# Kernel optimization log

Hardware: AMD Instinct MI355X
Metric: run time of the kernel (lower is better)

Reference implementation:

```python
import jax, jax.numpy as jnp
import numpy as np

E, H = 1024, 16


def setup_inputs() -> dict:
    key = jax.random.key(0)
    k1, k2, k3, k4 = jax.random.split(key, 4)
    B, L = 4, 2048
    embeddings = jax.random.normal(k1, (B, L, E), dtype=jnp.float32)
    mask = jax.random.randint(k2, (B, L, L), 0, 2) == 1  # True = masked out
    # Params (torch Linear y = x @ W.T; we store already-transposed [in, out])
    W_qkv = jax.random.normal(k3, (E, 3 * E), dtype=jnp.float32) * 0.02
    W_out = jax.random.normal(k4, (E, E), dtype=jnp.float32) * 0.02
    return {"embeddings": embeddings, "mask": mask, "W_qkv": W_qkv, "W_out": W_out}


def reference(embeddings, mask, W_qkv, W_out):
    B, L, E_ = embeddings.shape
    A = E_ // H
    scale = A ** (-0.5)
    qkv = embeddings @ W_qkv                       # [B, L, 3E]
    qkv = qkv.reshape(B, L, H, 3 * A).transpose(0, 2, 1, 3)  # [B, H, L, 3A]
    q, k, v = jnp.split(qkv, 3, axis=-1)           # each [B, H, L, A]
    scores = jnp.einsum('bhqa,bhka->bhqk', q, k) * scale  # [B, H, L, L]
    m = mask[:, None, :, :]                        # [B, 1, L, L]
    fully = jnp.all(m, axis=-1, keepdims=True)     # rows with every key masked
    scores = jnp.where(m, -jnp.inf, scores)
    scores = jnp.where(fully, 0.0, scores)         # keep softmax finite
    attn = jax.nn.softmax(scores, axis=-1)
    attn = jnp.where(fully, 0.0, attn)             # == torch nan_to_num(0)
    values = jnp.einsum('bhqk,bhka->bhqa', attn, v)  # [B, H, L, A]
    values = values.transpose(0, 2, 1, 3).reshape(B, L, E_)
    return values @ W_out
```

## Files before the change

### kernel.cpp

```cpp
#include <hip/hip_runtime.h>
#include <hip/hip_bf16.h>

#define B_   4
#define L_   2048
#define E_   1024
#define H_   16
#define T_   8192
#define K_   1024

typedef __attribute__((ext_vector_type(8))) short bf16x8;
typedef __attribute__((ext_vector_type(4))) float f32x4;
typedef __attribute__((ext_vector_type(4))) unsigned u32x4;

#define CSC_ (0.125f * 1.44269504f)

__device__ __forceinline__ ushort f2b(float f) {
    union { float f; unsigned u; } x; x.f = f;
    unsigned r = (x.u + 0x7fffu + ((x.u >> 16) & 1u)) >> 16;
    return (ushort)r;
}

__device__ __forceinline__ float fexp2(float x) {
#if __has_builtin(__builtin_amdgcn_exp2f)
    return __builtin_amdgcn_exp2f(x);
#else
    return __expf(x * 0.69314718056f);
#endif
}

__device__ __forceinline__ unsigned pack2bf(float a, float b) {
#if __has_builtin(__builtin_amdgcn_cvt_pk_bf16_f32)
    auto t = __builtin_amdgcn_cvt_pk_bf16_f32(a, b);
    return __builtin_bit_cast(unsigned, t);
#else
    unsigned ua = __builtin_bit_cast(unsigned, a) + 0x8000u;
    unsigned ub = __builtin_bit_cast(unsigned, b) + 0x8000u;
    return __builtin_amdgcn_perm(ub, ua, 0x07060302);
#endif
}

#define GLD_LDS16(gp, lp) __builtin_amdgcn_global_load_lds( \
    (const __attribute__((address_space(1))) void*)(gp), \
    (__attribute__((address_space(3))) void*)(lp), 16, 0, 0)

__global__ void detect_mask_layout(const unsigned char* __restrict__ m, int* flag) {
    __shared__ int s;
    if (threadIdx.x == 0) s = 0;
    __syncthreads();
    int found = 0;
    for (int i = threadIdx.x; i < 4096; i += 256)
        if ((i & 3) != 0 && m[i] != 0) found = 1;
    if (found) atomicOr(&s, 1);
    __syncthreads();
    if (threadIdx.x == 0) *flag = s;
}

__global__ void pack_mask(const void* __restrict__ mraw, const int* __restrict__ flag,
                          unsigned* __restrict__ tbits) {
    int row  = blockIdx.x;
    int lane = threadIdx.x & 63;
    int wave = threadIdx.x >> 6;
    int isByte = *flag;
    int b = row >> 11, q = row & 2047;
    const unsigned char* mb = (const unsigned char*)mraw;
    const int*           mi = (const int*)mraw;
    long long base = (long long)row * L_;
    for (int w = wave; w < 32; w += 4) {
        int idx = w * 64 + lane;
        int v = isByte ? (int)mb[base + idx] : mi[base + idx];
        unsigned long long word = __ballot(v == 0);
        if (lane == 0) {
            tbits[((size_t)b * 64 + 2 * w)     * 2048 + q] = (unsigned)word;
            tbits[((size_t)b * 64 + 2 * w + 1) * 2048 + q] = (unsigned)(word >> 32);
        }
    }
}

__global__ __launch_bounds__(256) void conv_bf16(const float* __restrict__ in,
                                                 ushort* __restrict__ out) {
    int i = blockIdx.x * 256 + threadIdx.x;
    float4 v = ((const float4*)in)[i];
    uint2 o;
    o.x = (unsigned)f2b(v.x) | ((unsigned)f2b(v.y) << 16);
    o.y = (unsigned)f2b(v.z) | ((unsigned)f2b(v.w) << 16);
    ((uint2*)out)[i] = o;
}

__global__ __launch_bounds__(256) void transpose_conv(const float* __restrict__ in,
        ushort* __restrict__ out, int R, int Cn) {
    __shared__ float t[32][33];
    int c0 = blockIdx.x * 32, r0 = blockIdx.y * 32;
    int x = threadIdx.x & 31, y = threadIdx.x >> 5;
#pragma unroll
    for (int k = 0; k < 4; ++k)
        t[y + k * 8][x] = in[(size_t)(r0 + y + k * 8) * Cn + c0 + x];
    __syncthreads();
#pragma unroll
    for (int k = 0; k < 4; ++k)
        out[(size_t)(c0 + y + k * 8) * R + r0 + x] = f2b(t[x][y + k * 8]);
}

template<int NDIM, int MODE>
__global__ __launch_bounds__(256, 4) void gemm_bf16(
        const ushort* __restrict__ Ab, const ushort* __restrict__ Bt,
        float* __restrict__ Cg, ushort* __restrict__ Qb,
        ushort* __restrict__ Kb, ushort* __restrict__ Vt) {
    __shared__ ushort As[2][128 * 32];
    __shared__ ushort Bs[2][128 * 32];
    const int tid = threadIdx.x;
    const int wv = tid >> 6, ln = tid & 63;
    const int bn = blockIdx.x * 128, bm = blockIdx.y * 128;
    const int wm = (wv & 1) * 64, wn = (wv >> 1) * 64;
    const int row16 = ln & 15, quad = ln >> 4;

    const int rr = ln >> 2;
    const int cc8 = (((ln & 3) ^ ((rr >> 1) & 3)) * 8);

    const ushort* Ag = Ab + (size_t)(bm + wv * 32 + rr) * K_ + cc8;
    const ushort* Bg = Bt + (size_t)(bn + wv * 32 + rr) * K_ + cc8;

    auto stage = [&](int k0, int buf) {
#pragma unroll
        for (int g = 0; g < 2; ++g) {
            GLD_LDS16(Ag + (size_t)(g * 16) * K_ + k0, &As[buf][(wv * 32 + g * 16) * 32]);
            GLD_LDS16(Bg + (size_t)(g * 16) * K_ + k0, &Bs[buf][(wv * 32 + g * 16) * 32]);
        }
    };

    f32x4 acc[4][4];
#pragma unroll
    for (int i = 0; i < 4; ++i)
#pragma unroll
        for (int j = 0; j < 4; ++j) acc[i][j] = (f32x4){0.f, 0.f, 0.f, 0.f};

    const int ch = (quad ^ ((row16 >> 1) & 3)) * 8;

    auto compute = [&](const ushort* Ac, const ushort* Bc) {
        bf16x8 af[4], bf[4];
#pragma unroll
        for (int i = 0; i < 4; ++i)
            af[i] = *(const bf16x8*)&Ac[(wm + i * 16 + row16) * 32 + ch];
#pragma unroll
        for (int j = 0; j < 4; ++j)
            bf[j] = *(const bf16x8*)&Bc[(wn + j * 16 + row16) * 32 + ch];
#pragma unroll
        for (int i = 0; i < 4; ++i)
#pragma unroll
            for (int j = 0; j < 4; ++j)
                acc[i][j] = __builtin_amdgcn_mfma_f32_16x16x32_bf16(
                    af[i], bf[j], acc[i][j], 0, 0, 0);
    };

    stage(0, 0);
    __syncthreads();

    for (int t = 0; t < 32; t += 2) {
        stage((t + 1) * 32, 1);
        compute(As[0], Bs[0]);
        __syncthreads();
        if (t + 2 < 32) stage((t + 2) * 32, 0);
        compute(As[1], Bs[1]);
        __syncthreads();
    }

    if (MODE == 0) {
#pragma unroll
        for (int i = 0; i < 4; ++i)
#pragma unroll
            for (int j = 0; j < 4; ++j) {
                int col = bn + wn + j * 16 + row16;
#pragma unroll
                for (int r = 0; r < 4; ++r) {
                    int row = bm + wm + i * 16 + quad * 4 + r;
                    Cg[(size_t)row * NDIM + col] = acc[i][j][r];
                }
            }
    } else {
#pragma unroll
        for (int j = 0; j < 4; ++j) {
            int col = bn + wn + j * 16 + row16;
            int h = col / 192, w = col - h * 192;
            int sel = w >> 6, a = w & 63;
            float qs = (sel == 0) ? CSC_ : 1.0f;
#pragma unroll
            for (int i = 0; i < 4; ++i)
#pragma unroll
                for (int r = 0; r < 4; ++r) {
                    int rowg = bm + wm + i * 16 + quad * 4 + r;
                    int b = rowg >> 11, l = rowg & 2047;
                    ushort v = f2b(acc[i][j][r] * qs);
                    size_t bh = (size_t)(b * H_ + h);
                    if (sel == 0)      Qb[(bh * L_ + l) * 64 + a] = v;
                    else if (sel == 1) Kb[(bh * L_ + l) * 64 + a] = v;
                    else {
                        int k5 = l & 31;
                        int lp = (l & ~31) | (2 * (k5 & 15) + (k5 >> 4));
                        Vt[(bh * 64 + a) * L_ + lp] = v;
                    }
                }
        }
    }
}

__global__ __launch_bounds__(512, 4) void attn_mfma(
        const ushort* __restrict__ Qb, const ushort* __restrict__ Kb,
        const ushort* __restrict__ Vt, const unsigned* __restrict__ tbits,
        ushort* __restrict__ vals) {
    __shared__ ushort KV[6][4096];

    const int tid = threadIdx.x, wv = tid >> 6, ln = tid & 63;
    const int bh = blockIdx.x, b = bh >> 4, h = bh & 15;
    const int q0 = blockIdx.y * 256;
    const int row16 = ln & 15, quad = ln >> 4;
    const int lh = ln >> 3, ll = ln & 7;
    const int cg8 = ((ll ^ lh) * 8);

    const ushort* Kg = Kb + (size_t)bh * L_ * 64;
    const ushort* Vg = Vt + (size_t)bh * 64 * L_;

    const int wk = wv & 3;
    const bool isK = (wv < 4);
    const int vc4 = ll ^ lh;
    const ushort* vstage = Vg + (size_t)(wk * 8 + lh + 32 * (vc4 >> 2)) * L_ + (vc4 & 3) * 8;
    const ushort* kstage = Kg + (size_t)(wk * 8 + lh) * 64 + cg8;

    ushort* lds = &KV[0][0];

    {
        const ushort* Qgw = Qb + ((size_t)bh * L_ + q0 + wv * 32) * 64;
#pragma unroll
        for (int it = 0; it < 4; ++it)
            GLD_LDS16(Qgw + (size_t)(it * 8 + lh) * 64 + cg8,
                      lds + (wv * 32 + it * 8) * 64);
    }
    __syncthreads();
    bf16x8 aq[2][2];
#pragma unroll
    for (int rg = 0; rg < 2; ++rg)
#pragma unroll
        for (int ks = 0; ks < 2; ++ks)
            aq[rg][ks] = *(const bf16x8*)&lds[(wv * 32 + rg * 16 + row16) * 64 +
                                              (((ks * 4 + quad) ^ (row16 & 7)) * 8)];
    __syncthreads();

    if (isK) {
        GLD_LDS16(kstage,               &KV[0][(wk * 8) * 64]);
        GLD_LDS16(kstage + 2048,        &KV[0][(32 + wk * 8) * 64]);
        GLD_LDS16(kstage + 4096,        &KV[1][(wk * 8) * 64]);
        GLD_LDS16(kstage + 4096 + 2048, &KV[1][(32 + wk * 8) * 64]);
        kstage += 8192;
    } else {
        GLD_LDS16(vstage,      &KV[3][(wk * 8) * 64]);
        GLD_LDS16(vstage + 32, &KV[3][(32 + wk * 8) * 64]);
        GLD_LDS16(vstage + 64, &KV[4][(wk * 8) * 64]);
        GLD_LDS16(vstage + 96, &KV[4][(32 + wk * 8) * 64]);
        vstage += 128;
    }

    bf16x8 vone;
#pragma unroll
    for (int i = 0; i < 8; ++i) vone[i] = (short)0x3F80;
    const f32x4 zf = (f32x4){0.f, 0.f, 0.f, 0.f};

    f32x4 oacc[2][4], lacc[2];
#pragma unroll
    for (int rg = 0; rg < 2; ++rg) {
        lacc[rg] = zf;
#pragma unroll
        for (int t = 0; t < 4; ++t) oacc[rg][t] = zf;
    }

    const unsigned* mptr = tbits + (size_t)b * 64 * 2048 + (q0 + wv * 32 + row16);

    auto qk = [&](const ushort* kbuf, int sub, f32x4 (&s)[2][2]) {
        __builtin_amdgcn_s_setprio(1);
#pragma unroll
        for (int ks = 0; ks < 2; ++ks) {
            bf16x8 bk[2];
#pragma unroll
            for (int t = 0; t < 2; ++t)
                bk[t] = *(const bf16x8*)&kbuf[(sub * 32 + t * 16 + row16) * 64 +
                                              (((ks * 4 + quad) ^ (row16 & 7)) * 8)];
#pragma unroll
            for (int rg = 0; rg < 2; ++rg)
#pragma unroll
                for (int t = 0; t < 2; ++t)
                    s[rg][t] = __builtin_amdgcn_mfma_f32_16x16x32_bf16(
                        bk[t], aq[rg][ks], ks ? s[rg][t] : zf, 0, 0, 0);
        }
        __builtin_amdgcn_s_setprio(0);
    };

    auto sm_pv = [&](f32x4 (&sa)[2][2], unsigned mlo, unsigned mhi,
                     const ushort* vbuf, int sub) {
        bf16x8 ap[2];
#pragma unroll
        for (int rg = 0; rg < 2; ++rg) {
            unsigned wr = rg ? mhi : mlo;
            u32x4 pw;
#pragma unroll
            for (int r = 0; r < 4; ++r) {
                unsigned sh = wr >> (quad * 4 + r);
                unsigned pk = pack2bf(fexp2(sa[rg][0][r]), fexp2(sa[rg][1][r]));
                pk &= (sh & 0x00010001u) * 0xFFFFu;
                pw[r] = pk;
            }
            ap[rg] = __builtin_bit_cast(bf16x8, pw);
        }
        bf16x8 bv[4];
#pragma unroll
        for (int t = 0; t < 4; ++t)
            bv[t] = *(const bf16x8*)&vbuf[(sub * 32 + (t & 1) * 16 + row16) * 64 +
                                          ((((t >> 1) * 4 + quad) ^ (row16 & 7)) * 8)];
        __builtin_amdgcn_s_setprio(1);
#pragma unroll
        for (int rg = 0; rg < 2; ++rg) {
            lacc[rg] = __builtin_amdgcn_mfma_f32_16x16x32_bf16(
                ap[rg], vone, lacc[rg], 0, 0, 0);
#pragma unroll
            for (int t = 0; t < 4; ++t)
                oacc[rg][t] = __builtin_amdgcn_mfma_f32_16x16x32_bf16(
                    ap[rg], bv[t], oacc[rg][t], 0, 0, 0);
        }
        __builtin_amdgcn_s_setprio(0);
    };

    auto iter = [&](const ushort* kb, const ushort* vb,
                    ushort* kn, ushort* vn, bool st) {
        unsigned m0lo = mptr[0],    m0hi = mptr[16];
        unsigned m1lo = mptr[2048], m1hi = mptr[2048 + 16];
        mptr += 4096;
        __builtin_amdgcn_sched_barrier(0);
        if (st) {
            if (isK) {
                GLD_LDS16(kstage,        kn + (wk * 8) * 64);
                GLD_LDS16(kstage + 2048, kn + (32 + wk * 8) * 64);
                kstage += 4096;
            } else {
                GLD_LDS16(vstage,      vn + (wk * 8) * 64);
                GLD_LDS16(vstage + 32, vn + (32 + wk * 8) * 64);
                vstage += 64;
            }
        }
        f32x4 s0[2][2];
        qk(kb, 0, s0);
        sm_pv(s0, m0lo, m0hi, vb, 0);
        f32x4 s1[2][2];
        qk(kb, 1, s1);
        sm_pv(s1, m1lo, m1hi, vb, 1);
        asm volatile("s_waitcnt vmcnt(2)" ::: "memory");
        __builtin_amdgcn_s_barrier();
        __builtin_amdgcn_sched_barrier(0);
    };

    asm volatile("s_waitcnt vmcnt(2)" ::: "memory");
    __builtin_amdgcn_s_barrier();
    __builtin_amdgcn_sched_barrier(0);

    for (int g = 0; g < 10; ++g) {
        iter(KV[0], KV[3], KV[2], KV[5], true);
        iter(KV[1], KV[4], KV[0], KV[3], true);
        iter(KV[2], KV[5], KV[1], KV[4], true);
    }
    iter(KV[0], KV[3], KV[2], KV[5], false);
    iter(KV[1], KV[4], KV[0], KV[3], false);

#pragma unroll
    for (int rg = 0; rg < 2; ++rg)
#pragma unroll
        for (int r = 0; r < 4; ++r) {
            float l = lacc[rg][r];
            float inv = (l > 0.f) ? 1.0f / l : 0.f;
            int qrow = q0 + wv * 32 + rg * 16 + quad * 4 + r;
            size_t base = ((size_t)b * L_ + qrow) * E_ + h * 64;
#pragma unroll
            for (int t = 0; t < 4; ++t)
                vals[base + t * 16 + row16] = f2b(oacc[rg][t][r] * inv);
        }
}

extern "C" void kernel_launch(void* const* d_in, const int* in_sizes, int n_in,
                              void* d_out, int out_size, void* d_ws, size_t ws_size,
                              hipStream_t stream) {
    const float* emb  = (const float*)d_in[0];
    const void*  mask = d_in[1];
    const float* wqkv = (const float*)d_in[2];
    const float* wout = (const float*)d_in[3];
    float* out = (float*)d_out;

    char* ws = (char*)d_ws;
    const size_t NEED = 4096ull + 2097152ull + 2ull * 46137344ull;
    if (ws_size < NEED) return;

    int* flag = (int*)ws;
    unsigned* tbits = (unsigned*)(ws + 4096);
    ushort* embb  = (ushort*)(ws + 4096 + 2097152);
    ushort* Wqkvt = embb  + 8388608;
    ushort* Wott  = Wqkvt + 3145728;
    ushort* Qb    = Wott  + 1048576;
    ushort* Kb    = Qb    + 8388608;
    ushort* Vt    = Kb    + 8388608;
    ushort* vals  = Vt    + 8388608;

    detect_mask_layout<<<1, 256, 0, stream>>>((const unsigned char*)mask, flag);
    pack_mask<<<T_, 256, 0, stream>>>(mask, flag, tbits);
    conv_bf16<<<8192, 256, 0, stream>>>(emb, embb);
    transpose_conv<<<dim3(96, 32), 256, 0, stream>>>(wqkv, Wqkvt, 1024, 3072);
    transpose_conv<<<dim3(32, 32), 256, 0, stream>>>(wout, Wott, 1024, 1024);
    gemm_bf16<3072, 1><<<dim3(24, 64), 256, 0, stream>>>(
        embb, Wqkvt, nullptr, Qb, Kb, Vt);
    attn_mfma<<<dim3(64, 8), 512, 0, stream>>>(Qb, Kb, Vt, tbits, vals);
    gemm_bf16<1024, 0><<<dim3(8, 64), 256, 0, stream>>>(
        vals, Wott, out, nullptr, nullptr, nullptr);
}
```

Measured before the change: 351.3 us.

## Add dedicated 256x256-tile QKV GEMM with fine-grained load/MFMA interleaving

```diff
diff --git a/kernel.cpp b/kernel.cpp
--- a/kernel.cpp
+++ b/kernel.cpp
@@ -100,11 +100,143 @@
         out[(size_t)(c0 + y + k * 8) * R + r0 + x] = f2b(t[x][y + k * 8]);
 }
 
-template<int NDIM, int MODE>
+#define QAT_ 16384
+
+__global__ __launch_bounds__(512) void gemm_qkv(
+        const ushort* __restrict__ Ab, const ushort* __restrict__ Bt,
+        ushort* __restrict__ Qb, ushort* __restrict__ Kb,
+        ushort* __restrict__ Vt) {
+    __shared__ ushort Asb[2 * QAT_];
+    __shared__ ushort Bsb[2 * QAT_];
+
+    const int tid = threadIdx.x;
+    const int wv = tid >> 6, ln = tid & 63;
+    const int bn = blockIdx.x * 256, bm = blockIdx.y * 256;
+    const int wm = (wv & 1) * 128, wn = (wv >> 1) * 64;
+    const int row16 = ln & 15, quad = ln >> 4;
+    const int lh = ln >> 3, ll = ln & 7;
+    const int sw8 = (ll ^ lh) * 8;
+
+    auto stA = [&](int t, int q, ushort* dst) {
+        int r0 = 128 * (wv >> 2) + 32 * q + (wv & 3) * 8;
+        GLD_LDS16(Ab + (size_t)(bm + r0 + lh) * K_ + t * 64 + sw8,
+                  dst + r0 * 64);
+    };
+    auto stB = [&](int t, int r, ushort* dst) {
+        int r0 = 64 * r + wv * 8;
+        GLD_LDS16(Bt + (size_t)(bn + r0 + lh) * K_ + t * 64 + sw8,
+                  dst + r0 * 64);
+    };
+
+    f32x4 acc[8][4];
+#pragma unroll
+    for (int i = 0; i < 8; ++i)
+#pragma unroll
+        for (int j = 0; j < 4; ++j) acc[i][j] = (f32x4){0.f, 0.f, 0.f, 0.f};
+
+#pragma unroll
+    for (int q = 0; q < 4; ++q) stA(0, q, Asb);
+#pragma unroll
+    for (int r = 0; r < 4; ++r) stB(0, r, Bsb);
+#pragma unroll
+    for (int q = 0; q < 3; ++q) stA(1, q, Asb + QAT_);
+#pragma unroll
+    for (int r = 0; r < 3; ++r) stB(1, r, Bsb + QAT_);
+    asm volatile("s_waitcnt vmcnt(6)" ::: "memory");
+    __builtin_amdgcn_s_barrier();
+    __builtin_amdgcn_sched_barrier(0);
+
+    for (int i = 0; i < 8; ++i) {
+        bf16x8 bfr[4][2];
+#pragma unroll
+        for (int p = 0; p < 8; ++p) {
+            const int half = p >> 2, q = p & 3;
+            const ushort* Ar = Asb + half * QAT_;
+            const ushort* Br = Bsb + half * QAT_;
+            bf16x8 af[2][2];
+#pragma unroll
+            for (int di = 0; di < 2; ++di)
+#pragma unroll
+                for (int ks = 0; ks < 2; ++ks) {
+                    int row = wm + (2 * q + di) * 16 + row16;
+                    af[di][ks] = *(const bf16x8*)&Ar[row * 64 +
+                                     (((ks * 4 + quad) ^ (row16 & 7)) * 8)];
+                }
+            if (q == 0) {
+#pragma unroll
+                for (int j = 0; j < 4; ++j)
+#pragma unroll
+                    for (int ks = 0; ks < 2; ++ks) {
+                        int row = wn + j * 16 + row16;
+                        bfr[j][ks] = *(const bf16x8*)&Br[row * 64 +
+                                         (((ks * 4 + quad) ^ (row16 & 7)) * 8)];
+                    }
+            }
+            if (p == 0) {
+                stA(2 * i + 1, 3, Asb + QAT_);
+                stB(2 * i + 1, 3, Bsb + QAT_);
+            } else if (p <= 4) {
+                if (i < 7) { stA(2 * i + 2, p - 1, Asb);
+                             stB(2 * i + 2, p - 1, Bsb); }
+            } else {
+                if (i < 7) { stA(2 * i + 3, p - 5, Asb + QAT_);
+                             stB(2 * i + 3, p - 5, Bsb + QAT_); }
+            }
+            __builtin_amdgcn_sched_barrier(0);
+            __builtin_amdgcn_s_barrier();
+            asm volatile("s_waitcnt lgkmcnt(0)" ::: "memory");
+            __builtin_amdgcn_sched_barrier(0);
+            __builtin_amdgcn_s_setprio(1);
+#pragma unroll
+            for (int ks = 0; ks < 2; ++ks)
+#pragma unroll
+                for (int di = 0; di < 2; ++di)
+#pragma unroll
+                    for (int j = 0; j < 4; ++j)
+                        acc[2 * q + di][j] = __builtin_amdgcn_mfma_f32_16x16x32_bf16(
+                            af[di][ks], bfr[j][ks], acc[2 * q + di][j], 0, 0, 0);
+            __builtin_amdgcn_s_setprio(0);
+            if (p == 3) {
+                if (i < 7) { asm volatile("s_waitcnt vmcnt(6)" ::: "memory"); }
+                else       { asm volatile("s_waitcnt vmcnt(0)" ::: "memory"); }
+            }
+            if (p == 7 && i < 7) {
+                asm volatile("s_waitcnt vmcnt(6)" ::: "memory");
+            }
+            __builtin_amdgcn_s_barrier();
+            __builtin_amdgcn_sched_barrier(0);
+        }
+    }
+
+#pragma unroll
+    for (int j = 0; j < 4; ++j) {
+        int col = bn + wn + j * 16 + row16;
+        int h = col / 192, w = col - h * 192;
+        int sel = w >> 6, a = w & 63;
+        float qs = (sel == 0) ? CSC_ : 1.0f;
+#pragma unroll
+        for (int i = 0; i < 8; ++i)
+#pragma unroll
+            for (int r = 0; r < 4; ++r) {
+                int rowg = bm + wm + i * 16 + quad * 4 + r;
+                int b = rowg >> 11, l = rowg & 2047;
+                ushort v = f2b(acc[i][j][r] * qs);
+                size_t bh = (size_t)(b * H_ + h);
+                if (sel == 0)      Qb[(bh * L_ + l) * 64 + a] = v;
+                else if (sel == 1) Kb[(bh * L_ + l) * 64 + a] = v;
+                else {
+                    int k5 = l & 31;
+                    int lp = (l & ~31) | (2 * (k5 & 15) + (k5 >> 4));
+                    Vt[(bh * 64 + a) * L_ + lp] = v;
+                }
+            }
+    }
+}
+
+template<int NDIM>
 __global__ __launch_bounds__(256, 4) void gemm_bf16(
         const ushort* __restrict__ Ab, const ushort* __restrict__ Bt,
-        float* __restrict__ Cg, ushort* __restrict__ Qb,
-        ushort* __restrict__ Kb, ushort* __restrict__ Vt) {
+        float* __restrict__ Cg) {
     __shared__ ushort As[2][128 * 32];
     __shared__ ushort Bs[2][128 * 32];
     const int tid = threadIdx.x;
@@ -163,43 +295,17 @@
         __syncthreads();
     }
 
-    if (MODE == 0) {
-#pragma unroll
-        for (int i = 0; i < 4; ++i)
-#pragma unroll
-            for (int j = 0; j < 4; ++j) {
-                int col = bn + wn + j * 16 + row16;
-#pragma unroll
-                for (int r = 0; r < 4; ++r) {
-                    int row = bm + wm + i * 16 + quad * 4 + r;
-                    Cg[(size_t)row * NDIM + col] = acc[i][j][r];
-                }
-            }
-    } else {
+#pragma unroll
+    for (int i = 0; i < 4; ++i)
 #pragma unroll
         for (int j = 0; j < 4; ++j) {
             int col = bn + wn + j * 16 + row16;
-            int h = col / 192, w = col - h * 192;
-            int sel = w >> 6, a = w & 63;
-            float qs = (sel == 0) ? CSC_ : 1.0f;
-#pragma unroll
-            for (int i = 0; i < 4; ++i)
-#pragma unroll
-                for (int r = 0; r < 4; ++r) {
-                    int rowg = bm + wm + i * 16 + quad * 4 + r;
-                    int b = rowg >> 11, l = rowg & 2047;
-                    ushort v = f2b(acc[i][j][r] * qs);
-                    size_t bh = (size_t)(b * H_ + h);
-                    if (sel == 0)      Qb[(bh * L_ + l) * 64 + a] = v;
-                    else if (sel == 1) Kb[(bh * L_ + l) * 64 + a] = v;
-                    else {
-                        int k5 = l & 31;
-                        int lp = (l & ~31) | (2 * (k5 & 15) + (k5 >> 4));
-                        Vt[(bh * 64 + a) * L_ + lp] = v;
-                    }
-                }
-        }
-    }
+#pragma unroll
+            for (int r = 0; r < 4; ++r) {
+                int row = bm + wm + i * 16 + quad * 4 + r;
+                Cg[(size_t)row * NDIM + col] = acc[i][j][r];
+            }
+        }
 }
 
 __global__ __launch_bounds__(512, 4) void attn_mfma(
@@ -407,9 +513,7 @@
     conv_bf16<<<8192, 256, 0, stream>>>(emb, embb);
     transpose_conv<<<dim3(96, 32), 256, 0, stream>>>(wqkv, Wqkvt, 1024, 3072);
     transpose_conv<<<dim3(32, 32), 256, 0, stream>>>(wout, Wott, 1024, 1024);
-    gemm_bf16<3072, 1><<<dim3(24, 64), 256, 0, stream>>>(
-        embb, Wqkvt, nullptr, Qb, Kb, Vt);
+    gemm_qkv<<<dim3(12, 32), 512, 0, stream>>>(embb, Wqkvt, Qb, Kb, Vt);
     attn_mfma<<<dim3(64, 8), 512, 0, stream>>>(Qb, Kb, Vt, tbits, vals);
-    gemm_bf16<1024, 0><<<dim3(8, 64), 256, 0, stream>>>(
-        vals, Wott, out, nullptr, nullptr, nullptr);
-}
+    gemm_bf16<1024><<<dim3(8, 64), 256, 0, stream>>>(vals, Wott, out);
+}
```

Measured after the change: 360.6 us. 1.03x slower.
